# Kernel tuning notes

Hardware: AMD Instinct MI355X
Metric: run time of the kernel (lower is better)

## Reference

```python
import jax, jax.numpy as jnp
import numpy as np

B, S, E, A = 4, 4096, 512, 64

def setup_inputs() -> dict:
    key = jax.random.key(0)
    ks = jax.random.split(key, 9)
    return {
        "query": jax.random.normal(ks[0], (B, S, E), dtype=jnp.float32),
        "key":   jax.random.normal(ks[1], (B, S, E), dtype=jnp.float32),
        "value": jax.random.normal(ks[2], (B, S, E), dtype=jnp.float32),
        "Wq": jax.random.normal(ks[3], (E, A), dtype=jnp.float32) / np.sqrt(E),
        "bq": jax.random.normal(ks[4], (A,), dtype=jnp.float32) * 0.01,
        "Wk": jax.random.normal(ks[5], (E, A), dtype=jnp.float32) / np.sqrt(E),
        "bk": jax.random.normal(ks[6], (A,), dtype=jnp.float32) * 0.01,
        "Wv": jax.random.normal(ks[7], (E, A), dtype=jnp.float32) / np.sqrt(E),
        "bv": jax.random.normal(ks[8], (A,), dtype=jnp.float32) * 0.01,
        "look_ahead_mask": 1,
    }

def reference(query, key, value, Wq, bq, Wk, bk, Wv, bv, look_ahead_mask):
    # Linear projections (torch Linear: x @ W^T + b; here W stored as [in,out])
    q = query @ Wq + bq            # [B,S,A]
    k = key   @ Wk + bk            # [B,S,A]
    v = value @ Wv + bv            # [B,S,A]
    scale = jnp.sqrt(jnp.asarray(A, dtype=q.dtype))
    qk = jnp.einsum('bsa,bta->bst', q, k) / scale   # [B,S,S]
    if look_ahead_mask:
        # faithful to source: MULTIPLICATIVE tril mask (not additive -inf)
        tril = jnp.tril(jnp.ones((qk.shape[-1], qk.shape[-1]), dtype=qk.dtype))
        qk = qk * tril
    attn = jax.nn.softmax(qk, axis=-1)              # [B,S,S]
    return jnp.einsum('bst,bta->bsa', attn, v)       # [B,S,A]
```

## Files before the change

kernel.cpp:

```cpp
#include <hip/hip_runtime.h>
#include <cstdint>

constexpr int BB = 4, SS = 4096, EE = 512, AA = 64;
constexpr int NT = 64;
constexpr int NSL = 288;

typedef __bf16 bf16x8 __attribute__((ext_vector_type(8)));
typedef float  f32x4  __attribute__((ext_vector_type(4)));
typedef float  f4     __attribute__((ext_vector_type(4)));
typedef unsigned short u16x4 __attribute__((ext_vector_type(4)));
typedef unsigned short u16x8 __attribute__((ext_vector_type(8)));

#define MFMA16(a, b, c) __builtin_amdgcn_mfma_f32_16x16x32_bf16((a), (b), (c), 0, 0, 0)

typedef const void __attribute__((address_space(1))) gvoid_t;
typedef void __attribute__((address_space(3))) lvoid_t;
__device__ __forceinline__ void gload16(const void* g, void* l) {
    __builtin_amdgcn_global_load_lds((gvoid_t*)g, (lvoid_t*)l, 16, 0, 0);
}

__device__ __forceinline__ unsigned short f2bf(float x) {
    union { float f; unsigned u; } v; v.f = x;
    unsigned r = v.u + 0x7fffu + ((v.u >> 16) & 1u);
    return (unsigned short)(r >> 16);
}
__device__ __forceinline__ float bf2f(unsigned short h) {
    union { unsigned u; float f; } v; v.u = ((unsigned)h) << 16;
    return v.f;
}
__device__ __forceinline__ bf16x8 as_bf16x8(u16x8 u) {
    union { u16x8 u; bf16x8 b; } v; v.u = u; return v.b;
}

__global__ void split_w_kernel(const float* __restrict__ Wq,
                               const float* __restrict__ Wk,
                               const float* __restrict__ Wv,
                               unsigned short* __restrict__ wt_h,
                               unsigned short* __restrict__ wt_l) {
    int idx = blockIdx.x * blockDim.x + threadIdx.x;
    if (idx >= 3 * EE * AA) return;
    int t = idx / (EE * AA);
    int rem = idx - t * (EE * AA);
    int k = rem >> 6;
    int n = rem & 63;
    const float* W = (t == 0) ? Wq : (t == 1) ? Wk : Wv;
    float x = W[k * AA + n];
    unsigned short h = f2bf(x);
    unsigned short l = f2bf(x - bf2f(h));
    int o = (t * AA + n) * EE + k;
    wt_h[o] = h;
    wt_l[o] = l;
}

__launch_bounds__(256)
__global__ void proj_kernel(const float* __restrict__ Xq,
                            const float* __restrict__ Xk,
                            const float* __restrict__ Xv,
                            const float* __restrict__ bq,
                            const float* __restrict__ bk,
                            const float* __restrict__ bv,
                            const unsigned short* __restrict__ wt_h,
                            const unsigned short* __restrict__ wt_l,
                            unsigned short* __restrict__ q_hi,
                            unsigned short* __restrict__ q_lo,
                            unsigned short* __restrict__ kv) {
    const int t = blockIdx.y;
    const float* X    = (t == 0) ? Xq : (t == 1) ? Xk : Xv;
    const float* bias = (t == 0) ? bq : (t == 1) ? bk : bv;
    const int row0 = blockIdx.x * 128;
    const int tid = threadIdx.x;
    const int lane = tid & 63, w = tid >> 6;
    const int l15 = lane & 15, l4 = lane >> 4;

    __shared__ __align__(16) unsigned short xh[128 * 64];
    __shared__ __align__(16) unsigned short xl[128 * 64];
    __shared__ __align__(16) unsigned short wh[64 * 64];
    __shared__ __align__(16) unsigned short wl[64 * 64];

    f32x4 acc[2][4];
#pragma unroll
    for (int m = 0; m < 2; ++m)
#pragma unroll
        for (int j = 0; j < 4; ++j) acc[m][j] = (f32x4){0.f, 0.f, 0.f, 0.f};

    const unsigned short* wtH = wt_h + t * AA * EE;
    const unsigned short* wtL = wt_l + t * AA * EE;

    for (int kc0 = 0; kc0 < EE; kc0 += 64) {
#pragma unroll
        for (int i = 0; i < 8; ++i) {
            int e = tid + i * 256;
            int r = e >> 4, c4 = e & 15;
            f4 v = *(const f4*)(X + (size_t)(row0 + r) * EE + kc0 + c4 * 4);
            u16x4 h, l;
#pragma unroll
            for (int j = 0; j < 4; ++j) {
                unsigned short hh = f2bf(v[j]);
                h[j] = hh;
                l[j] = f2bf(v[j] - bf2f(hh));
            }
            int byte = (r * 128 + c4 * 8) ^ ((r & 7) << 4);
            *(u16x4*)((char*)xh + byte) = h;
            *(u16x4*)((char*)xl + byte) = l;
        }
#pragma unroll
        for (int i = 0; i < 2; ++i) {
            int e = tid + i * 256;
            int n = e >> 3, k8 = e & 7;
            u16x8 h = *(const u16x8*)(wtH + n * EE + kc0 + k8 * 8);
            u16x8 l = *(const u16x8*)(wtL + n * EE + kc0 + k8 * 8);
            int byte = (n * 128 + k8 * 16) ^ ((n & 7) << 4);
            *(u16x8*)((char*)wh + byte) = h;
            *(u16x8*)((char*)wl + byte) = l;
        }
        __syncthreads();

#pragma unroll
        for (int kc = 0; kc < 2; ++kc) {
            bf16x8 a_h[2], a_l[2], b_h[4], b_l[4];
#pragma unroll
            for (int m = 0; m < 2; ++m) {
                int r = w * 32 + m * 16 + l15;
                int byte = (r * 128 + kc * 64 + l4 * 16) ^ ((r & 7) << 4);
                a_h[m] = as_bf16x8(*(const u16x8*)((const char*)xh + byte));
                a_l[m] = as_bf16x8(*(const u16x8*)((const char*)xl + byte));
            }
#pragma unroll
            for (int j = 0; j < 4; ++j) {
                int n = j * 16 + l15;
                int byte = (n * 128 + kc * 64 + l4 * 16) ^ ((n & 7) << 4);
                b_h[j] = as_bf16x8(*(const u16x8*)((const char*)wh + byte));
                b_l[j] = as_bf16x8(*(const u16x8*)((const char*)wl + byte));
            }
#pragma unroll
            for (int m = 0; m < 2; ++m)
#pragma unroll
                for (int j = 0; j < 4; ++j) {
                    acc[m][j] = MFMA16(a_h[m], b_h[j], acc[m][j]);
                    acc[m][j] = MFMA16(a_h[m], b_l[j], acc[m][j]);
                    acc[m][j] = MFMA16(a_l[m], b_h[j], acc[m][j]);
                }
        }
        __syncthreads();
    }

#pragma unroll
    for (int m = 0; m < 2; ++m) {
#pragma unroll
        for (int j = 0; j < 4; ++j) {
            int n = j * 16 + l15;
            float bv_ = bias[n];
#pragma unroll
            for (int reg = 0; reg < 4; ++reg) {
                int r = w * 32 + m * 16 + l4 * 4 + reg;
                int g = row0 + r;
                float val = acc[m][j][reg] + bv_;
                unsigned short h = f2bf(val);
                unsigned short lo = f2bf(val - bf2f(h));
                if (t == 0) {
                    size_t o = (size_t)g * AA + n;
                    q_hi[o] = h; q_lo[o] = lo;
                } else if (t == 1) {
                    int bb = g >> 12, s = g & 4095;
                    int kt = s >> 6, tt = s & 63;
                    size_t o = ((size_t)(bb * NT + kt) << 14) +
                               (size_t)(((((n >> 5) * 4 + (tt >> 4)) * 64 +
                                          ((n >> 3) & 3) * 16 + (tt & 15)) << 3) + (n & 7));
                    kv[o] = h; kv[o + 4096] = lo;
                } else {
                    int bb = g >> 12, s = g & 4095;
                    int kt = s >> 6, tt = s & 63;
                    size_t o = ((size_t)(bb * NT + kt) << 14) + 8192 +
                               (size_t)(((((tt >> 5) * 4 + (n >> 4)) * 64 +
                                          ((tt >> 3) & 3) * 16 + (n & 15)) << 3) + (tt & 7));
                    kv[o] = h; kv[o + 4096] = lo;
                }
            }
        }
    }
}

__launch_bounds__(64)
__global__ void sufv_kernel(const unsigned short* __restrict__ kv,
                            float* __restrict__ sufv) {
    const int b = blockIdx.x >> 6;
    const int a = blockIdx.x & 63;
    const int t = threadIdx.x;
    __shared__ float sums[64];
    const size_t tb = ((size_t)(b * NT + t) << 14) + 8192;
    const int j = a >> 4, l15i = a & 15;
    float s = 0.f;
#pragma unroll
    for (int c2 = 0; c2 < 2; ++c2) {
#pragma unroll
        for (int l4i = 0; l4i < 4; ++l4i) {
            size_t off = tb + (((c2 * 4 + j) * 64 + l4i * 16 + l15i) << 3);
            u16x8 h = *(const u16x8*)(kv + off);
            u16x8 l = *(const u16x8*)(kv + off + 4096);
#pragma unroll
            for (int q = 0; q < 8; ++q) s += bf2f(h[q]) + bf2f(l[q]);
        }
    }
    sums[t] = s;
    __syncthreads();
    float suf = 0.f;
    for (int jj = t + 1; jj < 64; ++jj) suf += sums[jj];
    sufv[((size_t)(b * 64 + a)) * 64 + t] = suf;
}

__launch_bounds__(256)
__global__ void attn_chunk_kernel(const unsigned short* __restrict__ q_hi,
                                  const unsigned short* __restrict__ q_lo,
                                  const unsigned short* __restrict__ kv,
                                  float* __restrict__ facc_part,
                                  float* __restrict__ l_part) {
    const int bxr = (NSL - 1) - blockIdx.x;
    const int b = blockIdx.y;
    int g = 7;
    while (4 * g * (g + 1) > bxr) --g;
    const int r_ = bxr - 4 * g * (g + 1);
    const int q_ = (int)((float)r_ * (1.0f / (float)(g + 1)) + 1e-4f);
    const int i  = g * 8 + q_;
    const int c  = r_ - q_ * (g + 1);
    const int t_begin = c * 8;
    const int t_end   = (t_begin + 8 < i + 1) ? t_begin + 8 : i + 1;

    const int tid = threadIdx.x;
    const int lane = tid & 63, w = tid >> 6;
    const int l15 = lane & 15, l4 = lane >> 4;

    __shared__ __align__(16) unsigned short kvbuf[16384];
    __shared__ __align__(16) unsigned short plds[4][1024];

    bf16x8 qh[2], ql[2];
    {
        size_t qrow = (size_t)(b * SS + i * 64 + w * 16 + l15) * AA;
#pragma unroll
        for (int kc = 0; kc < 2; ++kc) {
            qh[kc] = as_bf16x8(*(const u16x8*)(q_hi + qrow + kc * 32 + l4 * 8));
            ql[kc] = as_bf16x8(*(const u16x8*)(q_lo + qrow + kc * 32 + l4 * 8));
        }
    }

    f32x4 facc[4];
#pragma unroll
    for (int j = 0; j < 4; ++j) facc[j] = (f32x4){0.f, 0.f, 0.f, 0.f};
    float lsum[4] = {0.f, 0.f, 0.f, 0.f};

    const char* lb = (const char*)kvbuf;

    for (int kt = t_begin; kt < t_end; ++kt) {
        {
            const char* gt = (const char*)kv + (((size_t)(b * NT + kt)) << 15) +
                             w * 8192 + lane * 16;
            char* lw = (char*)kvbuf + w * 8192;
#pragma unroll
            for (int s = 0; s < 8; ++s) gload16(gt + s * 1024, lw + s * 1024);
        }
        asm volatile("s_waitcnt vmcnt(0)" ::: "memory");
        __syncthreads();

        f32x4 sc[4];
#pragma unroll
        for (int j = 0; j < 4; ++j) sc[j] = (f32x4){0.f, 0.f, 0.f, 0.f};
#pragma unroll
        for (int kc = 0; kc < 2; ++kc) {
#pragma unroll
            for (int j2 = 0; j2 < 4; ++j2) {
                int f = kc * 4 + j2;
                bf16x8 h = as_bf16x8(*(const u16x8*)(lb + f * 1024 + lane * 16));
                bf16x8 l = as_bf16x8(*(const u16x8*)(lb + 8192 + f * 1024 + lane * 16));
                sc[j2] = MFMA16(qh[kc], h, sc[j2]);
                sc[j2] = MFMA16(qh[kc], l, sc[j2]);
                sc[j2] = MFMA16(ql[kc], h, sc[j2]);
            }
        }

        const bool diag = (kt == i);
        float pv[4][4];
#pragma unroll
        for (int j2 = 0; j2 < 4; ++j2) {
#pragma unroll
            for (int reg = 0; reg < 4; ++reg) {
                float s = sc[j2][reg] * 0.125f;
                if (diag) {
                    int qr = w * 16 + l4 * 4 + reg;
                    int tg = j2 * 16 + l15;
                    if (tg > qr) s = 0.f;
                }
                float p = __expf(s);
                pv[j2][reg] = p;
                lsum[reg] += p;
            }
        }
#pragma unroll
        for (int j2 = 0; j2 < 4; ++j2) {
#pragma unroll
            for (int reg = 0; reg < 4; ++reg) {
                int row = l4 * 4 + reg, col = j2 * 16 + l15;
                int byte = (row * 128 + col * 2) ^ ((row & 7) << 4);
                *(unsigned short*)((char*)plds[w] + byte) = f2bf(pv[j2][reg]);
            }
        }
#pragma unroll
        for (int c2 = 0; c2 < 2; ++c2) {
            int byteA = (l15 * 128 + c2 * 64 + l4 * 16) ^ ((l15 & 7) << 4);
            bf16x8 pf = as_bf16x8(*(const u16x8*)((const char*)plds[w] + byteA));
#pragma unroll
            for (int j = 0; j < 4; ++j) {
                int f = c2 * 4 + j;
                bf16x8 vh = as_bf16x8(*(const u16x8*)(lb + 16384 + f * 1024 + lane * 16));
                bf16x8 vl = as_bf16x8(*(const u16x8*)(lb + 24576 + f * 1024 + lane * 16));
                facc[j] = MFMA16(pf, vh, facc[j]);
                facc[j] = MFMA16(pf, vl, facc[j]);
            }
        }
        __syncthreads();
    }

#pragma unroll
    for (int reg = 0; reg < 4; ++reg) {
        float rs = lsum[reg];
#pragma unroll
        for (int off = 1; off < 16; off <<= 1) rs += __shfl_xor(rs, off);
        lsum[reg] = rs;
    }

    const size_t slot = (size_t)b * NSL + bxr;
    float* fp = facc_part + slot * 4096;
#pragma unroll
    for (int j = 0; j < 4; ++j) {
#pragma unroll
        for (int reg = 0; reg < 4; ++reg) {
            int row = w * 16 + l4 * 4 + reg, a = j * 16 + l15;
            fp[row * 64 + a] = facc[j][reg];
        }
    }
    if (l15 == 0) {
#pragma unroll
        for (int reg = 0; reg < 4; ++reg)
            l_part[slot * 64 + w * 16 + l4 * 4 + reg] = lsum[reg];
    }
}

__launch_bounds__(256)
__global__ void combine_kernel(const float* __restrict__ facc_part,
                               const float* __restrict__ l_part,
                               const float* __restrict__ sufv,
                               float* __restrict__ out) {
    const int i = blockIdx.x;
    const int b = blockIdx.y;
    const int tid = threadIdx.x;
    const int g = i >> 3;
    const int nch = g + 1;
    const size_t slot0 = (size_t)b * NSL + 4 * g * (g + 1) + (i & 7) * nch;
    __shared__ float linv[64];
    __shared__ float sv[64];
    if (tid < 64) {
        float l = (float)(64 * (NT - 1 - i));
        for (int cc = 0; cc < nch; ++cc) l += l_part[(slot0 + cc) * 64 + tid];
        linv[tid] = 1.f / l;
        sv[tid] = sufv[((size_t)(b * 64 + tid)) * 64 + i];
    }
    __syncthreads();
    float* ob = out + ((size_t)(b * SS + i * 64)) * AA;
#pragma unroll
    for (int k = 0; k < 4; ++k) {
        int e = (tid + k * 256) * 4;
        int row = e >> 6, a = e & 63;
        f4 acc = {sv[a], sv[a + 1], sv[a + 2], sv[a + 3]};
        for (int cc = 0; cc < nch; ++cc) {
            f4 v = *(const f4*)(facc_part + (slot0 + cc) * 4096 + e);
            acc += v;
        }
        acc *= linv[row];
        *(f4*)(ob + e) = acc;
    }
}

extern "C" void kernel_launch(void* const* d_in, const int* in_sizes, int n_in,
                              void* d_out, int out_size, void* d_ws, size_t ws_size,
                              hipStream_t stream) {
    const float* query = (const float*)d_in[0];
    const float* key   = (const float*)d_in[1];
    const float* value = (const float*)d_in[2];
    const float* Wq    = (const float*)d_in[3];
    const float* bq    = (const float*)d_in[4];
    const float* Wk    = (const float*)d_in[5];
    const float* bk    = (const float*)d_in[6];
    const float* Wv    = (const float*)d_in[7];
    const float* bv    = (const float*)d_in[8];

    char* ws = (char*)d_ws;
    const size_t MB = 1u << 20;
    unsigned short* q_hi = (unsigned short*)(ws + 0 * MB);
    unsigned short* q_lo = (unsigned short*)(ws + 2 * MB);
    unsigned short* kv   = (unsigned short*)(ws + 4 * MB);
    float* sufv      = (float*)(ws + 12 * MB);
    float* l_part    = (float*)(ws + 13 * MB);
    float* facc_part = (float*)(ws + 14 * MB);
    unsigned short* wt_h = (unsigned short*)(ws + 34 * MB);
    unsigned short* wt_l = wt_h + 3 * AA * EE;

    split_w_kernel<<<(3 * EE * AA + 255) / 256, 256, 0, stream>>>(Wq, Wk, Wv, wt_h, wt_l);
    proj_kernel<<<dim3(BB * SS / 128, 3), 256, 0, stream>>>(
        query, key, value, bq, bk, bv, wt_h, wt_l, q_hi, q_lo, kv);
    sufv_kernel<<<BB * AA, 64, 0, stream>>>(kv, sufv);
    attn_chunk_kernel<<<dim3(NSL, BB), 256, 0, stream>>>(
        q_hi, q_lo, kv, facc_part, l_part);
    combine_kernel<<<dim3(NT, BB), 256, 0, stream>>>(facc_part, l_part, sufv, (float*)d_out);
}
```

Measured before the change: 96.81 us.

## Drop LDS staging in projection kernel, load MFMA operands directly from global

The projection kernel no longer stages X and weight tiles through shared memory with barriers. Each wave now loads its 16 rows of X straight into registers in MFMA fragment order and splits them into bf16 hi/lo there, and it reads weight fragments directly from global memory. The block tile is halved to 64 rows, so the grid doubles. The aim is to remove LDS traffic and __syncthreads stalls and to raise occupancy. In exchange, each fp32 X load is 32 bytes per lane with row-strided access, and weights are re-read from global/L2 by every wave.

```diff
diff --git a/kernel.cpp b/kernel.cpp
--- a/kernel.cpp
+++ b/kernel.cpp
@@ -67,114 +67,79 @@
     const int t = blockIdx.y;
     const float* X    = (t == 0) ? Xq : (t == 1) ? Xk : Xv;
     const float* bias = (t == 0) ? bq : (t == 1) ? bk : bv;
-    const int row0 = blockIdx.x * 128;
+    const int row0 = blockIdx.x * 64;
     const int tid = threadIdx.x;
     const int lane = tid & 63, w = tid >> 6;
     const int l15 = lane & 15, l4 = lane >> 4;
 
-    __shared__ __align__(16) unsigned short xh[128 * 64];
-    __shared__ __align__(16) unsigned short xl[128 * 64];
-    __shared__ __align__(16) unsigned short wh[64 * 64];
-    __shared__ __align__(16) unsigned short wl[64 * 64];
-
-    f32x4 acc[2][4];
-#pragma unroll
-    for (int m = 0; m < 2; ++m)
-#pragma unroll
-        for (int j = 0; j < 4; ++j) acc[m][j] = (f32x4){0.f, 0.f, 0.f, 0.f};
+    f32x4 acc[4];
+#pragma unroll
+    for (int j = 0; j < 4; ++j) acc[j] = (f32x4){0.f, 0.f, 0.f, 0.f};
 
     const unsigned short* wtH = wt_h + t * AA * EE;
     const unsigned short* wtL = wt_l + t * AA * EE;
 
-    for (int kc0 = 0; kc0 < EE; kc0 += 64) {
-#pragma unroll
-        for (int i = 0; i < 8; ++i) {
-            int e = tid + i * 256;
-            int r = e >> 4, c4 = e & 15;
-            f4 v = *(const f4*)(X + (size_t)(row0 + r) * EE + kc0 + c4 * 4);
-            u16x4 h, l;
-#pragma unroll
-            for (int j = 0; j < 4; ++j) {
-                unsigned short hh = f2bf(v[j]);
-                h[j] = hh;
-                l[j] = f2bf(v[j] - bf2f(hh));
-            }
-            int byte = (r * 128 + c4 * 8) ^ ((r & 7) << 4);
-            *(u16x4*)((char*)xh + byte) = h;
-            *(u16x4*)((char*)xl + byte) = l;
-        }
-#pragma unroll
-        for (int i = 0; i < 2; ++i) {
-            int e = tid + i * 256;
-            int n = e >> 3, k8 = e & 7;
-            u16x8 h = *(const u16x8*)(wtH + n * EE + kc0 + k8 * 8);
-            u16x8 l = *(const u16x8*)(wtL + n * EE + kc0 + k8 * 8);
-            int byte = (n * 128 + k8 * 16) ^ ((n & 7) << 4);
-            *(u16x8*)((char*)wh + byte) = h;
-            *(u16x8*)((char*)wl + byte) = l;
-        }
-        __syncthreads();
-
-#pragma unroll
-        for (int kc = 0; kc < 2; ++kc) {
-            bf16x8 a_h[2], a_l[2], b_h[4], b_l[4];
-#pragma unroll
-            for (int m = 0; m < 2; ++m) {
-                int r = w * 32 + m * 16 + l15;
-                int byte = (r * 128 + kc * 64 + l4 * 16) ^ ((r & 7) << 4);
-                a_h[m] = as_bf16x8(*(const u16x8*)((const char*)xh + byte));
-                a_l[m] = as_bf16x8(*(const u16x8*)((const char*)xl + byte));
-            }
-#pragma unroll
-            for (int j = 0; j < 4; ++j) {
-                int n = j * 16 + l15;
-                int byte = (n * 128 + kc * 64 + l4 * 16) ^ ((n & 7) << 4);
-                b_h[j] = as_bf16x8(*(const u16x8*)((const char*)wh + byte));
-                b_l[j] = as_bf16x8(*(const u16x8*)((const char*)wl + byte));
-            }
-#pragma unroll
-            for (int m = 0; m < 2; ++m)
-#pragma unroll
-                for (int j = 0; j < 4; ++j) {
-                    acc[m][j] = MFMA16(a_h[m], b_h[j], acc[m][j]);
-                    acc[m][j] = MFMA16(a_h[m], b_l[j], acc[m][j]);
-                    acc[m][j] = MFMA16(a_l[m], b_h[j], acc[m][j]);
-                }
-        }
-        __syncthreads();
-    }
-
-#pragma unroll
-    for (int m = 0; m < 2; ++m) {
+    const float* xrow = X + (size_t)(row0 + w * 16 + l15) * EE + l4 * 8;
+    int woff0 = (0 * 16 + l15) * EE + l4 * 8;
+    int woff1 = (1 * 16 + l15) * EE + l4 * 8;
+    int woff2 = (2 * 16 + l15) * EE + l4 * 8;
+    int woff3 = (3 * 16 + l15) * EE + l4 * 8;
+
+#pragma unroll 2
+    for (int kq = 0; kq < 16; ++kq) {
+        const int k0 = kq * 32;
+        f4 v0 = *(const f4*)(xrow + k0);
+        f4 v1 = *(const f4*)(xrow + k0 + 4);
+        u16x8 ahu, alu;
+#pragma unroll
+        for (int jj = 0; jj < 4; ++jj) {
+            unsigned short h0 = f2bf(v0[jj]);
+            ahu[jj] = h0;
+            alu[jj] = f2bf(v0[jj] - bf2f(h0));
+            unsigned short h1 = f2bf(v1[jj]);
+            ahu[jj + 4] = h1;
+            alu[jj + 4] = f2bf(v1[jj] - bf2f(h1));
+        }
+        bf16x8 a_h = as_bf16x8(ahu), a_l = as_bf16x8(alu);
 #pragma unroll
         for (int j = 0; j < 4; ++j) {
-            int n = j * 16 + l15;
-            float bv_ = bias[n];
-#pragma unroll
-            for (int reg = 0; reg < 4; ++reg) {
-                int r = w * 32 + m * 16 + l4 * 4 + reg;
-                int g = row0 + r;
-                float val = acc[m][j][reg] + bv_;
-                unsigned short h = f2bf(val);
-                unsigned short lo = f2bf(val - bf2f(h));
-                if (t == 0) {
-                    size_t o = (size_t)g * AA + n;
-                    q_hi[o] = h; q_lo[o] = lo;
-                } else if (t == 1) {
-                    int bb = g >> 12, s = g & 4095;
-                    int kt = s >> 6, tt = s & 63;
-                    size_t o = ((size_t)(bb * NT + kt) << 14) +
-                               (size_t)(((((n >> 5) * 4 + (tt >> 4)) * 64 +
-                                          ((n >> 3) & 3) * 16 + (tt & 15)) << 3) + (n & 7));
-                    kv[o] = h; kv[o + 4096] = lo;
-                } else {
-                    int bb = g >> 12, s = g & 4095;
-                    int kt = s >> 6, tt = s & 63;
-                    size_t o = ((size_t)(bb * NT + kt) << 14) + 8192 +
-                               (size_t)(((((tt >> 5) * 4 + (n >> 4)) * 64 +
-                                          ((tt >> 3) & 3) * 16 + (n & 15)) << 3) + (tt & 7));
-                    kv[o] = h; kv[o + 4096] = lo;
-                }
+            int wo = (j == 0) ? woff0 : (j == 1) ? woff1 : (j == 2) ? woff2 : woff3;
+            bf16x8 b_h = as_bf16x8(*(const u16x8*)(wtH + wo + k0));
+            bf16x8 b_l = as_bf16x8(*(const u16x8*)(wtL + wo + k0));
+            acc[j] = MFMA16(a_h, b_h, acc[j]);
+            acc[j] = MFMA16(a_h, b_l, acc[j]);
+            acc[j] = MFMA16(a_l, b_h, acc[j]);
+        }
+    }
+
+#pragma unroll
+    for (int j = 0; j < 4; ++j) {
+        int n = j * 16 + l15;
+        float bv_ = bias[n];
+#pragma unroll
+        for (int reg = 0; reg < 4; ++reg) {
+            int r = w * 16 + l4 * 4 + reg;
+            int g = row0 + r;
+            float val = acc[j][reg] + bv_;
+            unsigned short h = f2bf(val);
+            unsigned short lo = f2bf(val - bf2f(h));
+            if (t == 0) {
+                size_t o = (size_t)g * AA + n;
+                q_hi[o] = h; q_lo[o] = lo;
+            } else if (t == 1) {
+                int bb = g >> 12, s = g & 4095;
+                int kt = s >> 6, tt = s & 63;
+                size_t o = ((size_t)(bb * NT + kt) << 14) +
+                           (size_t)(((((n >> 5) * 4 + (tt >> 4)) * 64 +
+                                      ((n >> 3) & 3) * 16 + (tt & 15)) << 3) + (n & 7));
+                kv[o] = h; kv[o + 4096] = lo;
+            } else {
+                int bb = g >> 12, s = g & 4095;
+                int kt = s >> 6, tt = s & 63;
+                size_t o = ((size_t)(bb * NT + kt) << 14) + 8192 +
+                           (size_t)(((((tt >> 5) * 4 + (n >> 4)) * 64 +
+                                      ((tt >> 3) & 3) * 16 + (n & 15)) << 3) + (tt & 7));
+                kv[o] = h; kv[o + 4096] = lo;
             }
         }
     }
@@ -403,7 +368,7 @@
     unsigned short* wt_l = wt_h + 3 * AA * EE;
 
     split_w_kernel<<<(3 * EE * AA + 255) / 256, 256, 0, stream>>>(Wq, Wk, Wv, wt_h, wt_l);
-    proj_kernel<<<dim3(BB * SS / 128, 3), 256, 0, stream>>>(
+    proj_kernel<<<dim3(BB * SS / 64, 3), 256, 0, stream>>>(
         query, key, value, bq, bk, bv, wt_h, wt_l, q_hi, q_lo, kv);
     sufv_kernel<<<BB * AA, 64, 0, stream>>>(kv, sufv);
     attn_chunk_kernel<<<dim3(NSL, BB), 256, 0, stream>>>(
```

Result: slower. 126.8 us (+30.9%).
